# Performance work log

Measured on AMD Instinct MI355X. Metric: run time of the kernel, lower is better.

The kernel has to match this reference:

```python
import jax, jax.numpy as jnp
import numpy as np

NQ = 4
PI_HALF = np.pi / 2
HAD = jnp.array([[1, 1], [1, -1]], dtype=jnp.complex64) / np.sqrt(2)
CNOT = jnp.array([[1, 0, 0, 0], [0, 1, 0, 0], [0, 0, 0, 1], [0, 0, 1, 0]], dtype=jnp.complex64)
_bits = (np.arange(2 ** NQ)[:, None] >> np.arange(NQ - 1, -1, -1)[None, :]) & 1
ZSIGNS = jnp.asarray(1.0 - 2.0 * _bits, jnp.float32)  # [16, NQ]


def _ry(theta):
    c = jnp.cos(theta / 2).astype(jnp.complex64)
    s = jnp.sin(theta / 2).astype(jnp.complex64)
    return jnp.stack([jnp.stack([c, -s], -1), jnp.stack([s, c], -1)], -2)  # [...,2,2]


def _rot(phi, theta, omega):
    # PennyLane Rot = RZ(omega) @ RY(theta) @ RZ(phi)
    c = jnp.cos(theta / 2).astype(jnp.complex64)
    s = jnp.sin(theta / 2).astype(jnp.complex64)
    ep = jnp.exp(0.5j * phi).astype(jnp.complex64)
    eo = jnp.exp(0.5j * omega).astype(jnp.complex64)
    return jnp.stack([jnp.stack([jnp.conj(ep) * jnp.conj(eo) * c, -ep * jnp.conj(eo) * s]),
                      jnp.stack([jnp.conj(ep) * eo * s, ep * eo * c])])


def _cry(theta):
    # controlled-RY, batched: [B] -> [B,4,4], basis order (control, target)
    B = theta.shape[0]
    U = jnp.zeros((B, 4, 4), jnp.complex64).at[:, 0, 0].set(1.0).at[:, 1, 1].set(1.0)
    return U.at[:, 2:, 2:].set(_ry(theta))


def _apply1(state, U, wire):
    s = jnp.moveaxis(state, wire + 1, 1)
    shp = s.shape
    s = s.reshape(shp[0], 2, -1)
    s = jnp.einsum('ij,bjk->bik', U, s) if U.ndim == 2 else jnp.einsum('bij,bjk->bik', U, s)
    return jnp.moveaxis(s.reshape(shp), 1, wire + 1)


def _apply2(state, U, q0, q1):
    s = jnp.moveaxis(state, (q0 + 1, q1 + 1), (1, 2))
    shp = s.shape
    s = s.reshape(shp[0], 4, -1)
    s = jnp.einsum('ij,bjk->bik', U, s) if U.ndim == 2 else jnp.einsum('bij,bjk->bik', U, s)
    return jnp.moveaxis(s.reshape(shp), (1, 2), (q0 + 1, q1 + 1))


def _init_state(B):
    s = jnp.zeros((B, 2 ** NQ), jnp.complex64).at[:, 0].set(1.0)
    return s.reshape((B,) + (2,) * NQ)


def _zexp(state):
    p = state.reshape(state.shape[0], -1)
    p = p.real ** 2 + p.imag ** 2
    return p @ ZSIGNS  # [B, NQ]


def _attention_circuit(q, k, params):
    # q, k: [E, NQ] angles; params: [NQ, 3] shared
    s = _init_state(q.shape[0])
    for i in range(NQ):
        s = _apply1(s, _ry(q[:, i]), i)
    for i in range(NQ):
        s = _apply1(s, HAD, i)
    for i in range(NQ):
        s = _apply2(s, _cry(k[:, i]), i, (i + 1) % NQ)
    for i in range(NQ):
        s = _apply1(s, _rot(params[i, 0], params[i, 1], params[i, 2]), i)
    return _zexp(s)


def _entangle_circuit(x, params):
    # x: [N, NQ] angles; params: [n_layers, NQ, 3]
    s = _init_state(x.shape[0])
    for i in range(NQ):
        s = _apply1(s, _ry(x[:, i]), i)
    for l in range(params.shape[0]):
        for i in range(NQ - 1):
            s = _apply2(s, CNOT, i, i + 1)
        for i in range(NQ):
            s = _apply1(s, _rot(params[l, i, 0], params[l, i, 1], params[l, i, 2]), i)
        s = _apply2(s, CNOT, 0, NQ - 1)  # n_qubits >= 4
    return _zexp(s)


def _path_circuit(x, params):
    # x: [N, NQ]; params: [3, NQ, 3]
    s = _init_state(x.shape[0])
    for i in range(NQ):
        s = _apply1(s, HAD, i)
    for i in range(NQ):
        s = _apply1(s, _ry(x[:, i]), i)
    for l in range(3):
        for i in range(NQ):
            s = _apply1(s, _rot(params[l, i, 0], params[l, i, 1], params[l, i, 2]), i)
        for i in range(NQ - 1):
            s = _apply2(s, CNOT, i, i + 1)
    return _zexp(s)


def _forward(x, W_in, b_in, lin_W, lin_b, qproj_W, qproj_b, ent_params,
             attq_W, attq_b, attk_W, attk_b, att_qp, path_params,
             path_in_W, path_in_b, path_out_W, path_out_b, out_W, out_b, edge_index):
    N = x.shape[0]
    loops = jnp.arange(N, dtype=edge_index.dtype)
    ei = jnp.concatenate([edge_index, jnp.stack([loops, loops])], axis=1)  # add_self_loops
    src, dst = ei[0], ei[1]
    h = jax.nn.relu(x @ W_in.T + b_in)
    for l in range(lin_W.shape[0]):
        x_cls = h @ lin_W[l].T + lin_b[l]
        xq = _entangle_circuit(jnp.tanh(h[:, :NQ]) * PI_HALF, ent_params[l])
        x_comb = x_cls + xq @ qproj_W[l].T + qproj_b[l]
        q = jnp.tanh(h @ attq_W[l].T + attq_b[l]) * PI_HALF
        k = jnp.tanh(h @ attk_W[l].T + attk_b[l]) * PI_HALF
        scores = _attention_circuit(q[src], k[dst], att_qp[l]).mean(axis=1)  # [E]
        att = jax.nn.softmax(scores)  # global softmax over all edges (faithful)
        h = jax.ops.segment_sum(att[:, None] * x_comb[src], dst, num_segments=N)
        h = jax.nn.relu(h)  # dropout is identity at eval
    pq = jnp.tanh(h @ path_in_W.T + path_in_b) * PI_HALF
    h = _path_circuit(pq, path_params) @ path_out_W.T + path_out_b
    return h @ out_W.T + out_b


def setup_inputs() -> dict:
    key = jax.random.key(0)
    ks = jax.random.split(key, 22)
    N, E, D_in, D_h, D_out, L = 20000, 300000, 64, 128, 32, 2
    w = lambda k, shape: jax.random.normal(k, shape, jnp.float32) * 0.1
    return {
        'x': jax.random.normal(ks[0], (N, D_in), jnp.float32),
        'W_in': w(ks[1], (D_h, D_in)), 'b_in': w(ks[2], (D_h,)),
        'lin_W': w(ks[3], (L, D_h, D_h)), 'lin_b': w(ks[4], (L, D_h)),
        'qproj_W': w(ks[5], (L, D_h, NQ)), 'qproj_b': w(ks[6], (L, D_h)),
        'ent_params': w(ks[7], (L, 2, NQ, 3)),
        'attq_W': w(ks[8], (L, NQ, D_h)), 'attq_b': w(ks[9], (L, NQ)),
        'attk_W': w(ks[10], (L, NQ, D_h)), 'attk_b': w(ks[11], (L, NQ)),
        'att_qp': w(ks[12], (L, NQ, 3)),
        'path_params': w(ks[13], (3, NQ, 3)),
        'path_in_W': w(ks[14], (NQ, D_h)), 'path_in_b': w(ks[15], (NQ,)),
        'path_out_W': w(ks[16], (D_h, NQ)), 'path_out_b': w(ks[17], (D_h,)),
        'out_W': w(ks[18], (D_out, D_h)), 'out_b': w(ks[19], (D_out,)),
        'edge_index': jax.random.randint(ks[20], (2, E), 0, N, dtype=jnp.int32),
    }


def reference(x, W_in, b_in, lin_W, lin_b, qproj_W, qproj_b, ent_params,
              attq_W, attq_b, attk_W, attk_b, att_qp, path_params,
              path_in_W, path_in_b, path_out_W, path_out_b, out_W, out_b, edge_index):
    return _forward(x, W_in, b_in, lin_W, lin_b, qproj_W, qproj_b, ent_params,
                    attq_W, attq_b, attk_W, attk_b, att_qp, path_params,
                    path_in_W, path_in_b, path_out_W, path_out_b, out_W, out_b, edge_index)
```

## Files before the change

kernel.cpp:

```cpp
#include <hip/hip_runtime.h>
#include <math.h>

#define PI_HALF 1.57079632679489662f

__device__ __forceinline__ float fast_tanh(float x) {
    float e = __expf(2.f * x);
    return 1.f - 2.f * __builtin_amdgcn_rcpf(e + 1.f);
}


__device__ __forceinline__ void prod_init(float sr[16],
        float c0, float s0, float c1, float s1,
        float c2, float s2, float c3, float s3) {
    float p2[4];
    p2[0] = c0 * c1; p2[1] = c0 * s1; p2[2] = s0 * c1; p2[3] = s0 * s1;
    float p3[8];
#pragma unroll
    for (int j = 0; j < 4; ++j) { p3[2 * j] = p2[j] * c2; p3[2 * j + 1] = p2[j] * s2; }
#pragma unroll
    for (int j = 0; j < 8; ++j) { sr[2 * j] = p3[j] * c3; sr[2 * j + 1] = p3[j] * s3; }
}

template<int M>
__device__ __forceinline__ void had_r(float sr[16]) {
    const float r = 0.70710678118654752f;
#pragma unroll
    for (int i = 0; i < 16; ++i) {
        if (i & M) continue;
        const int j = i | M;
        float ar = sr[i], br = sr[j];
        sr[i] = (ar + br) * r;
        sr[j] = (ar - br) * r;
    }
}

template<int MC, int MT>
__device__ __forceinline__ void cry_r(float sr[16], float c, float s) {
#pragma unroll
    for (int i = 0; i < 16; ++i) {
        if (!(i & MC) || (i & MT)) continue;
        const int j = i | MT;
        float ar = sr[i], br = sr[j];
        sr[i] = c * ar - s * br;
        sr[j] = s * ar + c * br;
    }
}

template<int MC, int MT>
__device__ __forceinline__ void cnot_r(float sr[16]) {
#pragma unroll
    for (int i = 0; i < 16; ++i) {
        if (!(i & MC) || (i & MT)) continue;
        const int j = i | MT;
        float t = sr[i]; sr[i] = sr[j]; sr[j] = t;
    }
}

template<int MC, int MT>
__device__ __forceinline__ void cnot_g(float sr[16], float si[16]) {
#pragma unroll
    for (int i = 0; i < 16; ++i) {
        if (!(i & MC) || (i & MT)) continue;
        const int j = i | MT;
        float tr = sr[i], ti = si[i];
        sr[i] = sr[j]; si[i] = si[j];
        sr[j] = tr;    si[j] = ti;
    }
}

template<int M>
__device__ __forceinline__ void rot_pre(float sr[16], float si[16], const float* __restrict__ u) {
    const float u00r = u[0], u00i = u[1], u01r = u[2], u01i = u[3];
    const float u10r = u[4], u10i = u[5], u11r = u[6], u11i = u[7];
#pragma unroll
    for (int i = 0; i < 16; ++i) {
        if (i & M) continue;
        const int j = i | M;
        float ar = sr[i], ai = si[i], br = sr[j], bi = si[j];
        sr[i] = u00r * ar - u00i * ai + u01r * br - u01i * bi;
        si[i] = u00r * ai + u00i * ar + u01r * bi + u01i * br;
        sr[j] = u10r * ar - u10i * ai + u11r * br - u11i * bi;
        si[j] = u10r * ai + u10i * ar + u11r * bi + u11i * br;
    }
}

template<int M>
__device__ __forceinline__ void rot_first(float sr[16], float si[16], const float* __restrict__ u) {
    const float u00r = u[0], u00i = u[1], u01r = u[2], u01i = u[3];
    const float u10r = u[4], u10i = u[5], u11r = u[6], u11i = u[7];
#pragma unroll
    for (int i = 0; i < 16; ++i) {
        if (i & M) continue;
        const int j = i | M;
        float ar = sr[i], br = sr[j];
        sr[i] = u00r * ar + u01r * br;
        si[i] = u00i * ar + u01i * br;
        sr[j] = u10r * ar + u11r * br;
        si[j] = u10i * ar + u11i * br;
    }
}

__device__ __forceinline__ void zexp_g(const float sr[16], const float si[16], float z[4]) {
    float p[16];
#pragma unroll
    for (int i = 0; i < 16; ++i) p[i] = sr[i] * sr[i] + si[i] * si[i];
    z[0] = z[1] = z[2] = z[3] = 0.f;
#pragma unroll
    for (int i = 0; i < 16; ++i) {
        z[0] += (i & 8) ? -p[i] : p[i];
        z[1] += (i & 4) ? -p[i] : p[i];
        z[2] += (i & 2) ? -p[i] : p[i];
        z[3] += (i & 1) ? -p[i] : p[i];
    }
}


__global__ void k_fsi(const float* __restrict__ entp, const float* __restrict__ attqp,
                      const float* __restrict__ pparm,
                      const float* __restrict__ outW, const float* __restrict__ outb,
                      const float* __restrict__ poW, const float* __restrict__ pob,
                      float* __restrict__ rotbuf, float* __restrict__ M,
                      float* __restrict__ v,
                      const float* __restrict__ x, const float* __restrict__ W,
                      const float* __restrict__ b, float* __restrict__ h,
                      int* __restrict__ cnt, float* __restrict__ sumexp, int N) {
    __shared__ float xs[32 * 64];
    const int bb = blockIdx.x;
    const int tid = threadIdx.x;
    {
        const int gid = bb * 256 + tid;
        const int T = gridDim.x * 256;
        for (int i = gid; i < N; i += T) cnt[i] = 0;
        if (gid < 4) sumexp[gid] = 0.f;
    }
    if (bb == 0) {
        const int t = tid;
        if (t < 36) {
            const float* p;
            if (t < 16)      p = entp  + t * 3;
            else if (t < 24) p = attqp + (t - 16) * 3;
            else             p = pparm + (t - 24) * 3;
            float phi = p[0], theta = p[1], omega = p[2];
            float st, ct; sincosf(0.5f * theta, &st, &ct);
            float sp, cp; sincosf(0.5f * (phi + omega), &sp, &cp);
            float sm, cm; sincosf(0.5f * (phi - omega), &sm, &cm);
            float* u = rotbuf + t * 8;
            u[0] =  ct * cp;  u[1] = -ct * sp;
            u[2] = -st * cm;  u[3] = -st * sm;
            u[4] =  st * cm;  u[5] = -st * sm;
            u[6] =  ct * cp;  u[7] =  ct * sp;
        } else if (t >= 64 && t < 192) {
            int t2 = t - 64;
            int o = t2 >> 2, i = t2 & 3;
            float acc = 0.f;
            for (int j = 0; j < 128; ++j) acc += outW[o * 128 + j] * poW[j * 4 + i];
            M[t2] = acc;
        } else if (t >= 192 && t < 224) {
            int o = t - 192;
            float acc = outb[o];
            for (int j = 0; j < 128; ++j) acc += outW[o * 128 + j] * pob[j];
            v[o] = acc;
        }
        return;
    }
    const int base = (bb - 1) * 32;
    for (int idx = tid; idx < 32 * 64; idx += 256) {
        int n = base + (idx >> 6);
        xs[idx] = (n < N) ? x[(size_t)n * 64 + (idx & 63)] : 0.f;
    }
    __syncthreads();
    const int lane = tid & 63;
    const int wv = tid >> 6;
    const int ch0 = lane, ch1 = lane + 64;
    float acc0[8], acc1[8];
#pragma unroll
    for (int n = 0; n < 8; ++n) { acc0[n] = 0.f; acc1[n] = 0.f; }
    const float4* w04 = (const float4*)(W + ch0 * 64);
    const float4* w14 = (const float4*)(W + ch1 * 64);
    for (int c4 = 0; c4 < 16; ++c4) {
        float4 wa = w04[c4];
        float4 wb = w14[c4];
#pragma unroll
        for (int n = 0; n < 8; ++n) {
            float4 hv = *(const float4*)&xs[(wv * 8 + n) * 64 + c4 * 4];
            acc0[n] += wa.x * hv.x + wa.y * hv.y + wa.z * hv.z + wa.w * hv.w;
            acc1[n] += wb.x * hv.x + wb.y * hv.y + wb.z * hv.z + wb.w * hv.w;
        }
    }
    const float b0 = b[ch0];
    const float b1 = b[ch1];
#pragma unroll
    for (int n = 0; n < 8; ++n) {
        int node = base + wv * 8 + n;
        if (node < N) {
            h[(size_t)node * 128 + ch0] = fmaxf(acc0[n] + b0, 0.f);
            h[(size_t)node * 128 + ch1] = fmaxf(acc1[n] + b1, 0.f);
        }
    }
}

__global__ void k_hist(const int* __restrict__ ei, int* __restrict__ cnt, int E, int EP) {
    int e = blockIdx.x * blockDim.x + threadIdx.x;
    if (e >= EP) return;
    int d_ = (e < E) ? ei[E + e] : e - E;
    atomicAdd(&cnt[d_], 1);
}

__global__ void k_scan(const int* __restrict__ cnt, int* __restrict__ off,
                       int* __restrict__ cur, int N) {
    __shared__ int tot[1024];
    const int t = threadIdx.x;
    const int chunk = (N + 1023) >> 10;
    const int s0 = t * chunk;
    const int s1 = min(s0 + chunk, N);
    int sum = 0;
    for (int i = s0; i < s1; ++i) sum += cnt[i];
    tot[t] = sum;
    __syncthreads();
    for (int d = 1; d < 1024; d <<= 1) {
        int v = (t >= d) ? tot[t - d] : 0;
        __syncthreads();
        tot[t] += v;
        __syncthreads();
    }
    int run = (t == 0) ? 0 : tot[t - 1];
    for (int i = s0; i < s1; ++i) {
        off[i] = run; cur[i] = run;
        run += cnt[i];
    }
}

__global__ void k_qke(const float* __restrict__ h,
                      const float* __restrict__ aqW, const float* __restrict__ aqb,
                      const float* __restrict__ akW, const float* __restrict__ akb,
                      const float* __restrict__ rotE2,
                      float* __restrict__ qbuf, float* __restrict__ kbuf,
                      float* __restrict__ xq, int N,
                      const float* __restrict__ sprev,
                      int fillb, int dotb, const int* __restrict__ ei,
                      int* __restrict__ cur, int* __restrict__ srcs,
                      int* __restrict__ inv, int E, int EP) {
    int bb = blockIdx.x;
    const int tid = threadIdx.x;
    if (bb < fillb) {
        int e = bb * 256 + tid;
        if (e < EP) {
            int s_, d_;
            if (e < E) { s_ = ei[e]; d_ = ei[E + e]; } else { s_ = d_ = e - E; }
            int pos = atomicAdd(&cur[d_], 1);
            srcs[pos] = s_;
            inv[e] = pos;
        }
        return;
    }
    bb -= fillb;
    const float scale = sprev ? __builtin_amdgcn_rcpf(sprev[0]) : 1.0f;
    if (bb < dotb) {
        const int t = bb * 256 + tid;
        const int node = t >> 3;
        if (node >= N) return;
        const int which = t & 7;
        const int qi = which & 3;
        const float4* h4 = (const float4*)(h + (size_t)node * 128);
        const float4* w4 = (const float4*)(((which < 4) ? aqW : akW) + qi * 128);
        float dot = (which < 4) ? aqb[qi] : akb[qi];
        for (int c4 = 0; c4 < 32; ++c4) {
            float4 hv = h4[c4];
            hv.x *= scale; hv.y *= scale; hv.z *= scale; hv.w *= scale;
            float4 w = w4[c4];
            dot += w.x * hv.x + w.y * hv.y + w.z * hv.z + w.w * hv.w;
        }
        float halfang = fast_tanh(dot) * (0.5f * PI_HALF);
        float s, c; __sincosf(halfang, &s, &c);
        float* dst = ((which < 4) ? qbuf : kbuf) + (size_t)node * 8 + qi * 2;
        dst[0] = c; dst[1] = s;
        return;
    }
    bb -= dotb;
    const int node = bb * 256 + tid;
    if (node >= N) return;
    float4 hv = *(const float4*)(h + (size_t)node * 128);
    hv.x *= scale; hv.y *= scale; hv.z *= scale; hv.w *= scale;
    float c0, s0, c1, s1, c2, s2, c3, s3;
    { float a = fast_tanh(hv.x) * (0.5f * PI_HALF); __sincosf(a, &s0, &c0); }
    { float a = fast_tanh(hv.y) * (0.5f * PI_HALF); __sincosf(a, &s1, &c1); }
    { float a = fast_tanh(hv.z) * (0.5f * PI_HALF); __sincosf(a, &s2, &c2); }
    { float a = fast_tanh(hv.w) * (0.5f * PI_HALF); __sincosf(a, &s3, &c3); }
    float sr[16], si[16];
    prod_init(sr, c0, s0, c1, s1, c2, s2, c3, s3);
    cnot_r<8, 4>(sr); cnot_r<4, 2>(sr); cnot_r<2, 1>(sr);
    rot_first<8>(sr, si, rotE2);
    rot_pre<4>(sr, si, rotE2 + 8);
    rot_pre<2>(sr, si, rotE2 + 16);
    rot_pre<1>(sr, si, rotE2 + 24);
    cnot_g<8, 1>(sr, si);
    cnot_g<8, 4>(sr, si); cnot_g<4, 2>(sr, si); cnot_g<2, 1>(sr, si);
    const float* P = rotE2 + 32;
    rot_pre<8>(sr, si, P);
    rot_pre<4>(sr, si, P + 8);
    rot_pre<2>(sr, si, P + 16);
    rot_pre<1>(sr, si, P + 24);
    cnot_g<8, 1>(sr, si);
    float z[4]; zexp_g(sr, si, z);
    *(float4*)&xq[(size_t)node * 4] = make_float4(z[0], z[1], z[2], z[3]);
}

#define HS_STRIDE 132
__global__ void k_linatt(const float* __restrict__ h, const float* __restrict__ xq,
                         const float* __restrict__ linW, const float* __restrict__ linb,
                         const float* __restrict__ qpW, const float* __restrict__ qpb,
                         float* __restrict__ xcomb, int N,
                         const float* __restrict__ sprev, int nb16,
                         const float* __restrict__ qb, const float* __restrict__ kb,
                         const int* __restrict__ ei, const float* __restrict__ RA,
                         const int* __restrict__ inv, float* __restrict__ escore,
                         float* __restrict__ sumexp, int E, int EP) {
    __shared__ float hs[16 * HS_STRIDE];
    __shared__ float red[2];
    const int tid = threadIdx.x;
    if (blockIdx.x >= nb16) {
        int e = (blockIdx.x - nb16) * 128 + tid;
        float ex = 0.f;
        if (e < EP) {
            int s_, d_;
            if (e < E) { s_ = ei[e]; d_ = ei[E + e]; } else { s_ = d_ = e - E; }
            float4 qa = *(const float4*)&qb[(size_t)s_ * 8];
            float4 qc = *(const float4*)&qb[(size_t)s_ * 8 + 4];
            float4 ka = *(const float4*)&kb[(size_t)d_ * 8];
            float4 kc = *(const float4*)&kb[(size_t)d_ * 8 + 4];
            float sr[16], si[16];
            prod_init(sr, qa.x, qa.y, qa.z, qa.w, qc.x, qc.y, qc.z, qc.w);
            had_r<8>(sr); had_r<4>(sr); had_r<2>(sr); had_r<1>(sr);
            cry_r<8, 4>(sr, ka.x, ka.y);
            cry_r<4, 2>(sr, ka.z, ka.w);
            cry_r<2, 1>(sr, kc.x, kc.y);
            cry_r<1, 8>(sr, kc.z, kc.w);
            rot_first<8>(sr, si, RA);
            rot_pre<4>(sr, si, RA + 8);
            rot_pre<2>(sr, si, RA + 16);
            rot_pre<1>(sr, si, RA + 24);
            float p0  = sr[0]  * sr[0]  + si[0]  * si[0];
            float p1  = sr[1]  * sr[1]  + si[1]  * si[1];
            float p2  = sr[2]  * sr[2]  + si[2]  * si[2];
            float p4  = sr[4]  * sr[4]  + si[4]  * si[4];
            float p8  = sr[8]  * sr[8]  + si[8]  * si[8];
            float p7  = sr[7]  * sr[7]  + si[7]  * si[7];
            float p11 = sr[11] * sr[11] + si[11] * si[11];
            float p13 = sr[13] * sr[13] + si[13] * si[13];
            float p14 = sr[14] * sr[14] + si[14] * si[14];
            float p15 = sr[15] * sr[15] + si[15] * si[15];
            float sc = (p0 - p15) + 0.5f * ((p1 + p2 + p4 + p8) - (p7 + p11 + p13 + p14));
            ex = __expf(sc);
            escore[inv[e]] = ex;
        }
        float wsum = ex;
#pragma unroll
        for (int d = 32; d; d >>= 1) wsum += __shfl_xor(wsum, d, 64);
        if ((tid & 63) == 0) red[tid >> 6] = wsum;
        __syncthreads();
        if (tid == 0) atomicAdd(sumexp, red[0] + red[1]);
        return;
    }
    const int base = blockIdx.x * 16;
    const float scale = sprev ? __builtin_amdgcn_rcpf(sprev[0]) : 1.0f;
    for (int idx = tid; idx < 16 * 32; idx += 128) {
        int n = idx >> 5, c4 = idx & 31;
        int node = base + n;
        float4 hv = (node < N) ? *(const float4*)&h[(size_t)node * 128 + c4 * 4]
                               : make_float4(0.f, 0.f, 0.f, 0.f);
        hv.x *= scale; hv.y *= scale; hv.z *= scale; hv.w *= scale;
        *(float4*)&hs[n * HS_STRIDE + c4 * 4] = hv;
    }
    __syncthreads();
    const int lane = tid & 63;
    const int nh = tid >> 6;
    const int ch0 = lane, ch1 = lane + 64;
    float acc0[8], acc1[8];
#pragma unroll
    for (int n = 0; n < 8; ++n) { acc0[n] = 0.f; acc1[n] = 0.f; }
    const float4* w04 = (const float4*)(linW + ch0 * 128);
    const float4* w14 = (const float4*)(linW + ch1 * 128);
    for (int c4 = 0; c4 < 32; ++c4) {
        float4 wa = w04[c4];
        float4 wb = w14[c4];
#pragma unroll
        for (int n = 0; n < 8; ++n) {
            float4 hv = *(const float4*)&hs[(nh * 8 + n) * HS_STRIDE + c4 * 4];
            acc0[n] += wa.x * hv.x + wa.y * hv.y + wa.z * hv.z + wa.w * hv.w;
            acc1[n] += wb.x * hv.x + wb.y * hv.y + wb.z * hv.z + wb.w * hv.w;
        }
    }
    const float b0 = linb[ch0] + qpb[ch0];
    const float b1 = linb[ch1] + qpb[ch1];
    const float q00 = qpW[ch0 * 4 + 0], q01 = qpW[ch0 * 4 + 1];
    const float q02 = qpW[ch0 * 4 + 2], q03 = qpW[ch0 * 4 + 3];
    const float q10 = qpW[ch1 * 4 + 0], q11 = qpW[ch1 * 4 + 1];
    const float q12 = qpW[ch1 * 4 + 2], q13 = qpW[ch1 * 4 + 3];
#pragma unroll
    for (int n = 0; n < 8; ++n) {
        const int nl = nh * 8 + n;
        const int node = base + nl;
        if (node < N) {
            float4 xv = *(const float4*)&xq[(size_t)node * 4];
            xcomb[(size_t)node * 128 + ch0] = acc0[n] + b0
                + q00 * xv.x + q01 * xv.y + q02 * xv.z + q03 * xv.w;
            xcomb[(size_t)node * 128 + ch1] = acc1[n] + b1
                + q10 * xv.x + q11 * xv.y + q12 * xv.z + q13 * xv.w;
        }
    }
}

__global__ void k_gather(const float* __restrict__ xcomb, const int* __restrict__ srcs,
                         const float* __restrict__ escore, const int* __restrict__ off,
                         const int* __restrict__ cnt, float* __restrict__ h) {
    __shared__ int sS[128];
    __shared__ float wS[128];
    const int b = blockIdx.x;
    const int tid = threadIdx.x;
    const int start = off[b];
    const int num = cnt[b];
    float acc = 0.f;
    for (int base = 0; base < num; base += 128) {
        int m = min(128, num - base);
        if (tid < m) {
            sS[tid] = srcs[start + base + tid];
            wS[tid] = escore[start + base + tid];
        }
        __syncthreads();
        int i = 0;
        for (; i + 8 <= m; i += 8) {
            float v0 = xcomb[(size_t)sS[i + 0] * 128 + tid];
            float v1 = xcomb[(size_t)sS[i + 1] * 128 + tid];
            float v2 = xcomb[(size_t)sS[i + 2] * 128 + tid];
            float v3 = xcomb[(size_t)sS[i + 3] * 128 + tid];
            float v4 = xcomb[(size_t)sS[i + 4] * 128 + tid];
            float v5 = xcomb[(size_t)sS[i + 5] * 128 + tid];
            float v6 = xcomb[(size_t)sS[i + 6] * 128 + tid];
            float v7 = xcomb[(size_t)sS[i + 7] * 128 + tid];
            acc += wS[i + 0] * v0; acc += wS[i + 1] * v1;
            acc += wS[i + 2] * v2; acc += wS[i + 3] * v3;
            acc += wS[i + 4] * v4; acc += wS[i + 5] * v5;
            acc += wS[i + 6] * v6; acc += wS[i + 7] * v7;
        }
        for (; i < m; ++i)
            acc += wS[i] * xcomb[(size_t)sS[i] * 128 + tid];
        __syncthreads();
    }
    h[(size_t)b * 128 + tid] = fmaxf(acc, 0.f);
}

__global__ void k_tail(const float* __restrict__ h, const float* __restrict__ piW,
                       const float* __restrict__ pib, const float* __restrict__ RP,
                       const float* __restrict__ M, const float* __restrict__ v,
                       const float* __restrict__ sprev,
                       float* __restrict__ out, int N) {
    __shared__ float pqS[64 * 8];
    __shared__ float zS[64 * 4];
    __shared__ float MS[128];
    __shared__ float vS[32];
    const int tid = threadIdx.x;
    const int base = blockIdx.x * 64;
    if (tid < 128) MS[tid] = M[tid];
    else if (tid < 160) vS[tid - 128] = v[tid - 128];
    const float invS = __builtin_amdgcn_rcpf(sprev[0]);
    {
        const int nl = tid >> 2, i = tid & 3;
        const int node = base + nl;
        if (node < N) {
            float raw = 0.f;
            const float4* w4 = (const float4*)(piW + i * 128);
            const float4* h4 = (const float4*)(h + (size_t)node * 128);
#pragma unroll 8
            for (int c4 = 0; c4 < 32; ++c4) {
                float4 w = w4[c4];
                float4 hv = h4[c4];
                raw += w.x * hv.x + w.y * hv.y + w.z * hv.z + w.w * hv.w;
            }
            float dot = pib[i] + invS * raw;
            float halfang = fast_tanh(dot) * (0.5f * PI_HALF);
            float s, c; __sincosf(halfang, &s, &c);
            pqS[nl * 8 + i * 2]     = c;
            pqS[nl * 8 + i * 2 + 1] = s;
        }
    }
    __syncthreads();
    if (tid < 64 && base + tid < N) {
        const float r = 0.70710678118654752f;
        float c0 = pqS[tid * 8 + 0], s0 = pqS[tid * 8 + 1];
        float c1 = pqS[tid * 8 + 2], s1 = pqS[tid * 8 + 3];
        float c2 = pqS[tid * 8 + 4], s2 = pqS[tid * 8 + 5];
        float c3 = pqS[tid * 8 + 6], s3 = pqS[tid * 8 + 7];
        float u0 = r * (c0 - s0), w0 = r * (c0 + s0);
        float u1 = r * (c1 - s1), w1 = r * (c1 + s1);
        float u2 = r * (c2 - s2), w2 = r * (c2 + s2);
        float u3 = r * (c3 - s3), w3 = r * (c3 + s3);
        float sr[16], si[16];
        prod_init(sr, u0, w0, u1, w1, u2, w2, u3, w3);
        rot_first<8>(sr, si, RP);
        rot_pre<4>(sr, si, RP + 8);
        rot_pre<2>(sr, si, RP + 16);
        rot_pre<1>(sr, si, RP + 24);
        cnot_g<8, 4>(sr, si); cnot_g<4, 2>(sr, si); cnot_g<2, 1>(sr, si);
#pragma unroll
        for (int l = 1; l < 3; ++l) {
            const float* P = RP + l * 32;
            rot_pre<8>(sr, si, P);
            rot_pre<4>(sr, si, P + 8);
            rot_pre<2>(sr, si, P + 16);
            rot_pre<1>(sr, si, P + 24);
            cnot_g<8, 4>(sr, si); cnot_g<4, 2>(sr, si); cnot_g<2, 1>(sr, si);
        }
        float z[4]; zexp_g(sr, si, z);
        zS[tid * 4 + 0] = z[0]; zS[tid * 4 + 1] = z[1];
        zS[tid * 4 + 2] = z[2]; zS[tid * 4 + 3] = z[3];
    }
    __syncthreads();
#pragma unroll
    for (int k = 0; k < 8; ++k) {
        int flat = k * 256 + tid;
        int nl = flat >> 5;
        int o = flat & 31;
        int node = base + nl;
        if (node < N) {
            out[(size_t)node * 32 + o] = vS[o]
                + MS[o * 4 + 0] * zS[nl * 4 + 0] + MS[o * 4 + 1] * zS[nl * 4 + 1]
                + MS[o * 4 + 2] * zS[nl * 4 + 2] + MS[o * 4 + 3] * zS[nl * 4 + 3];
        }
    }
}


extern "C" void kernel_launch(void* const* d_in, const int* in_sizes, int n_in,
                              void* d_out, int out_size, void* d_ws, size_t ws_size,
                              hipStream_t stream) {
    const float* x     = (const float*)d_in[0];
    const float* W_in  = (const float*)d_in[1];
    const float* b_in  = (const float*)d_in[2];
    const float* linW  = (const float*)d_in[3];
    const float* linb  = (const float*)d_in[4];
    const float* qpW   = (const float*)d_in[5];
    const float* qpb   = (const float*)d_in[6];
    const float* entp  = (const float*)d_in[7];
    const float* aqW   = (const float*)d_in[8];
    const float* aqb   = (const float*)d_in[9];
    const float* akW   = (const float*)d_in[10];
    const float* akb   = (const float*)d_in[11];
    const float* attqp = (const float*)d_in[12];
    const float* pparm = (const float*)d_in[13];
    const float* piW   = (const float*)d_in[14];
    const float* pib   = (const float*)d_in[15];
    const float* poW   = (const float*)d_in[16];
    const float* pob   = (const float*)d_in[17];
    const float* outW  = (const float*)d_in[18];
    const float* outb  = (const float*)d_in[19];
    const int*   ei    = (const int*)d_in[20];

    const int N  = in_sizes[0] / 64;
    const int E  = in_sizes[20] / 2;
    const int EP = E + N;

    float* ws     = (float*)d_ws;
    float* h      = ws;
    float* xcomb  = h      + (size_t)N * 128;
    float* qbuf   = xcomb  + (size_t)N * 128;
    float* kbuf   = qbuf   + (size_t)N * 8;
    float* escore = kbuf   + (size_t)N * 8;
    float* rotbuf = escore + EP;
    float* Mm     = rotbuf + 36 * 8;
    float* vv     = Mm + 128;
    int*   cnt    = (int*)(vv + 32);
    float* sumexp = (float*)(cnt + N);
    int*   off    = (int*)(sumexp + 4);
    int*   cur    = off + N;
    int*   srcs   = cur + N;
    int*   inv    = srcs + EP;
    float* xq     = (float*)(inv + EP);

    const float* rotE = rotbuf;
    const float* rotA = rotbuf + 128;
    const float* rotP = rotbuf + 192;

    const int nb16 = (N + 15) / 16;
    const int nb32 = (N + 31) / 32;
    const int ebl  = (EP + 255) / 256;
    const int ebl128 = (EP + 127) / 128;
    const int dotb = (N * 8 + 255) / 256;
    const int circb = (N + 255) / 256;

    k_fsi<<<nb32 + 1, 256, 0, stream>>>(entp, attqp, pparm, outW, outb, poW, pob,
                                        rotbuf, Mm, vv, x, W_in, b_in, h,
                                        cnt, sumexp, N);
    k_hist<<<ebl, 256, 0, stream>>>(ei, cnt, E, EP);
    k_scan<<<1, 1024, 0, stream>>>(cnt, off, cur, N);

    for (int l = 0; l < 2; ++l) {
        const int fillb = (l == 0) ? ebl : 0;
        const float* sprev = (l == 0) ? (const float*)nullptr
                                      : (const float*)(sumexp + 0);
        k_qke<<<fillb + dotb + circb, 256, 0, stream>>>(h,
            aqW + (size_t)l * 4 * 128, aqb + l * 4,
            akW + (size_t)l * 4 * 128, akb + l * 4,
            rotE + l * 64, qbuf, kbuf, xq, N, sprev,
            fillb, dotb, ei, cur, srcs, inv, E, EP);
        k_linatt<<<nb16 + ebl128, 128, 0, stream>>>(h, xq,
            linW + (size_t)l * 128 * 128, linb + l * 128,
            qpW + (size_t)l * 128 * 4, qpb + l * 128,
            xcomb, N, sprev, nb16,
            qbuf, kbuf, ei, rotA + l * 32, inv, escore, sumexp + l, E, EP);
        k_gather<<<N, 128, 0, stream>>>(xcomb, srcs, escore, off, cnt, h);
    }

    k_tail<<<(N + 63) / 64, 256, 0, stream>>>(h, piW, pib, rotP, Mm, vv,
                                              sumexp + 1, (float*)d_out, N);
}
```

Baseline: 361.8 us.

## Compute edge scores in CSR order and prefetch linear weights

The scan kernel now writes a destination array in CSR-sorted order, so the attention-score pass iterates over sorted slots and reads src/dst from CSR arrays. The inverse permutation is dropped, and scores are written contiguously instead of scattered through inv, which also improves locality of the key reads. The single-block scan now serially writes every destination index, which adds latency on one block. The linear-layer loop also software-prefetches the next weight float4s.

```diff
diff --git a/kernel.cpp b/kernel.cpp
--- a/kernel.cpp
+++ b/kernel.cpp
@@ -207,7 +207,7 @@
 }
 
 __global__ void k_scan(const int* __restrict__ cnt, int* __restrict__ off,
-                       int* __restrict__ cur, int N) {
+                       int* __restrict__ cur, int* __restrict__ dsts, int N) {
     __shared__ int tot[1024];
     const int t = threadIdx.x;
     const int chunk = (N + 1023) >> 10;
@@ -226,7 +226,9 @@
     int run = (t == 0) ? 0 : tot[t - 1];
     for (int i = s0; i < s1; ++i) {
         off[i] = run; cur[i] = run;
-        run += cnt[i];
+        int c = cnt[i];
+        for (int j = 0; j < c; ++j) dsts[run + j] = i;
+        run += c;
     }
 }
 
@@ -239,7 +241,7 @@
                       const float* __restrict__ sprev,
                       int fillb, int dotb, const int* __restrict__ ei,
                       int* __restrict__ cur, int* __restrict__ srcs,
-                      int* __restrict__ inv, int E, int EP) {
+                      int E, int EP) {
     int bb = blockIdx.x;
     const int tid = threadIdx.x;
     if (bb < fillb) {
@@ -249,7 +251,6 @@
             if (e < E) { s_ = ei[e]; d_ = ei[E + e]; } else { s_ = d_ = e - E; }
             int pos = atomicAdd(&cur[d_], 1);
             srcs[pos] = s_;
-            inv[e] = pos;
         }
         return;
     }
@@ -312,22 +313,23 @@
                          float* __restrict__ xcomb, int N,
                          const float* __restrict__ sprev, int nb16,
                          const float* __restrict__ qb, const float* __restrict__ kb,
-                         const int* __restrict__ ei, const float* __restrict__ RA,
-                         const int* __restrict__ inv, float* __restrict__ escore,
-                         float* __restrict__ sumexp, int E, int EP) {
+                         const float* __restrict__ RA,
+                         const int* __restrict__ srcs, const int* __restrict__ dsts,
+                         float* __restrict__ escore,
+                         float* __restrict__ sumexp, int EP) {
     __shared__ float hs[16 * HS_STRIDE];
     __shared__ float red[2];
     const int tid = threadIdx.x;
     if (blockIdx.x >= nb16) {
-        int e = (blockIdx.x - nb16) * 128 + tid;
+        int s = (blockIdx.x - nb16) * 128 + tid;
         float ex = 0.f;
-        if (e < EP) {
-            int s_, d_;
-            if (e < E) { s_ = ei[e]; d_ = ei[E + e]; } else { s_ = d_ = e - E; }
-            float4 qa = *(const float4*)&qb[(size_t)s_ * 8];
-            float4 qc = *(const float4*)&qb[(size_t)s_ * 8 + 4];
-            float4 ka = *(const float4*)&kb[(size_t)d_ * 8];
-            float4 kc = *(const float4*)&kb[(size_t)d_ * 8 + 4];
+        if (s < EP) {
+            int src = srcs[s];
+            int dst = dsts[s];
+            float4 qa = *(const float4*)&qb[(size_t)src * 8];
+            float4 qc = *(const float4*)&qb[(size_t)src * 8 + 4];
+            float4 ka = *(const float4*)&kb[(size_t)dst * 8];
+            float4 kc = *(const float4*)&kb[(size_t)dst * 8 + 4];
             float sr[16], si[16];
             prod_init(sr, qa.x, qa.y, qa.z, qa.w, qc.x, qc.y, qc.z, qc.w);
             had_r<8>(sr); had_r<4>(sr); had_r<2>(sr); had_r<1>(sr);
@@ -351,7 +353,7 @@
             float p15 = sr[15] * sr[15] + si[15] * si[15];
             float sc = (p0 - p15) + 0.5f * ((p1 + p2 + p4 + p8) - (p7 + p11 + p13 + p14));
             ex = __expf(sc);
-            escore[inv[e]] = ex;
+            escore[s] = ex;
         }
         float wsum = ex;
 #pragma unroll
@@ -380,15 +382,19 @@
     for (int n = 0; n < 8; ++n) { acc0[n] = 0.f; acc1[n] = 0.f; }
     const float4* w04 = (const float4*)(linW + ch0 * 128);
     const float4* w14 = (const float4*)(linW + ch1 * 128);
+    float4 wa = w04[0];
+    float4 wb = w14[0];
     for (int c4 = 0; c4 < 32; ++c4) {
-        float4 wa = w04[c4];
-        float4 wb = w14[c4];
+        const int nx = (c4 + 1) & 31;
+        float4 wan = w04[nx];
+        float4 wbn = w14[nx];
 #pragma unroll
         for (int n = 0; n < 8; ++n) {
             float4 hv = *(const float4*)&hs[(nh * 8 + n) * HS_STRIDE + c4 * 4];
             acc0[n] += wa.x * hv.x + wa.y * hv.y + wa.z * hv.z + wa.w * hv.w;
             acc1[n] += wb.x * hv.x + wb.y * hv.y + wb.z * hv.z + wb.w * hv.w;
         }
+        wa = wan; wb = wbn;
     }
     const float b0 = linb[ch0] + qpb[ch0];
     const float b1 = linb[ch1] + qpb[ch1];
@@ -573,8 +579,8 @@
     int*   off    = (int*)(sumexp + 4);
     int*   cur    = off + N;
     int*   srcs   = cur + N;
-    int*   inv    = srcs + EP;
-    float* xq     = (float*)(inv + EP);
+    int*   dsts   = srcs + EP;
+    float* xq     = (float*)(dsts + EP);
 
     const float* rotE = rotbuf;
     const float* rotA = rotbuf + 128;
@@ -591,7 +597,7 @@
                                         rotbuf, Mm, vv, x, W_in, b_in, h,
                                         cnt, sumexp, N);
     k_hist<<<ebl, 256, 0, stream>>>(ei, cnt, E, EP);
-    k_scan<<<1, 1024, 0, stream>>>(cnt, off, cur, N);
+    k_scan<<<1, 1024, 0, stream>>>(cnt, off, cur, dsts, N);
 
     for (int l = 0; l < 2; ++l) {
         const int fillb = (l == 0) ? ebl : 0;
@@ -601,12 +607,12 @@
             aqW + (size_t)l * 4 * 128, aqb + l * 4,
             akW + (size_t)l * 4 * 128, akb + l * 4,
             rotE + l * 64, qbuf, kbuf, xq, N, sprev,
-            fillb, dotb, ei, cur, srcs, inv, E, EP);
+            fillb, dotb, ei, cur, srcs, E, EP);
         k_linatt<<<nb16 + ebl128, 128, 0, stream>>>(h, xq,
             linW + (size_t)l * 128 * 128, linb + l * 128,
             qpW + (size_t)l * 128 * 4, qpb + l * 128,
             xcomb, N, sprev, nb16,
-            qbuf, kbuf, ei, rotA + l * 32, inv, escore, sumexp + l, E, EP);
+            qbuf, kbuf, rotA + l * 32, srcs, dsts, escore, sumexp + l, EP);
         k_gather<<<N, 128, 0, stream>>>(xcomb, srcs, escore, off, cnt, h);
     }
 
```

Result: slower. 447.2 us (+23.6%).
